# Kernel tuning notes

Hardware: AMD Instinct MI355X
Metric: run time of the kernel (lower is better)

Reference implementation:

```python
import jax, jax.numpy as jnp
import numpy as np

N_NODES = 100000
N_EDGES = 1600000
D_IN, D_HID, D_OUT = 128, 64, 16


def _glorot(key, shape):
    lim = float(np.sqrt(6.0 / (shape[0] + shape[1])))
    return jax.random.uniform(key, shape, jnp.float32, -lim, lim)


def setup_inputs() -> dict:
    key = jax.random.key(0)
    k1, k2, k3 = jax.random.split(key, 3)
    x = jax.random.normal(k1, (N_NODES, D_IN), dtype=jnp.float32)
    edge_index = jax.random.randint(k2, (2, N_EDGES), 0, N_NODES, dtype=jnp.int64)
    kw1, kw2 = jax.random.split(k3)
    W1 = _glorot(kw1, (D_IN, D_HID))
    b1 = jnp.zeros((D_HID,), jnp.float32)
    W2 = _glorot(kw2, (D_HID, D_OUT))
    b2 = jnp.zeros((D_OUT,), jnp.float32)
    return {"x": x, "edge_index": edge_index, "W1": W1, "b1": b1, "W2": W2, "b2": b2}


def _gcn_conv(h, W, b, src, dst, norm, n_nodes):
    # PyG GCNConv: linear first, then normalized neighbor aggregation, then bias.
    h = h @ W                                        # [N, d_out]
    msg = h[src] * norm[:, None]                     # gather over edges(+self loops)
    out = jax.ops.segment_sum(msg, dst, num_segments=n_nodes)  # scatter-add
    return out + b


def reference(x, edge_index, W1, b1, W2, b2):
    n = x.shape[0]
    loop = jnp.arange(n, dtype=edge_index.dtype)
    src = jnp.concatenate([edge_index[0], loop])     # add self loops
    dst = jnp.concatenate([edge_index[1], loop])
    # symmetric normalization D^-1/2 (A+I) D^-1/2
    deg = jax.ops.segment_sum(jnp.ones(src.shape[0], x.dtype), dst, num_segments=n)
    dinv = jnp.where(deg > 0, jax.lax.rsqrt(jnp.maximum(deg, 1e-12)), 0.0)
    norm = dinv[src] * dinv[dst]                     # [E+N]

    out = _gcn_conv(x, W1, b1, src, dst, norm, n)
    out = jax.nn.sigmoid(out)
    # dropout p=0.5 with training=False -> identity (eval mode)
    out = _gcn_conv(out, W2, b2, src, dst, norm, n)
    return jax.nn.log_softmax(out, axis=1)
```

## Files before the change

### kernel.cpp

```cpp
#include <hip/hip_runtime.h>
#include <hip/hip_bf16.h>


constexpr int D_IN  = 128;
constexpr int D_HID = 64;
constexpr int D_OUT = 16;

constexpr int WSHIFT  = 9;
constexpr int MAXB    = 256;
constexpr int BCAP    = 12288;
constexpr int CSRCAP  = 16384;
constexpr int BIN_CAP = 48;
constexpr int CHUNK   = 4096;

typedef __attribute__((ext_vector_type(8))) short bf16x8;
typedef __attribute__((ext_vector_type(4))) float f32x4;

__device__ inline float bflo(unsigned u){ return __uint_as_float(u << 16); }
__device__ inline float bfhi(unsigned u){ return __uint_as_float(u & 0xffff0000u); }
__device__ inline unsigned f2bu(float f){
    __hip_bfloat16 h = __float2bfloat16(f);
    return (unsigned)*reinterpret_cast<unsigned short*>(&h);
}
__device__ inline float sigf(float x){ return 1.0f / (1.0f + __expf(-x)); }

__global__ __launch_bounds__(256) void k_bucketize(
    const int* __restrict__ ei, const unsigned* __restrict__ xraw,
    int* __restrict__ flags, unsigned* __restrict__ gcur,
    unsigned* __restrict__ gbuf, int ne, int B)
{
    __shared__ unsigned bcnt[MAXB];
    __shared__ unsigned bbase[MAXB];
    __shared__ unsigned bins[MAXB * BIN_CAP];
    __shared__ int s_i64;

    const int t = threadIdx.x, lane = t & 63, wv = t >> 6;
    const int e0 = blockIdx.x * CHUNK;

    if (t < MAXB) bcnt[t] = 0u;
    if (wv == 0){
        int w = ei[2 * lane + 1];
        unsigned long long m = __ballot(w == 0);
        if (lane == 0) s_i64 = (__popcll(m) > 48) ? 1 : 0;
        if (blockIdx.x == 0){
            unsigned u = xraw[lane];
            unsigned h0 = u & 0xffffu, h1 = u >> 16;
            unsigned ex0 = (h0 >> 7) & 0xffu, ex1 = (h1 >> 7) & 0xffu;
            bool bad0 = !((h0 & 0x7fffu) == 0 || (ex0 >= 97 && ex0 <= 157));
            bool bad1 = !((h1 & 0x7fffu) == 0 || (ex1 >= 97 && ex1 <= 157));
            unsigned long long m0 = __ballot(bad0);
            unsigned long long m1 = __ballot(bad1);
            if (lane == 0){
                int bad = __popcll(m0) + __popcll(m1);
                flags[0] = (bad > 8) ? 0 : 1;
                flags[1] = s_i64;
            }
        }
    }
    __syncthreads();
    const int i64 = s_i64;
    const bool vec = ((ne & 1) == 0);

    #pragma unroll
    for (int k = 0; k < CHUNK / 512; ++k){
        int e = e0 + k * 512 + 2 * t;
        int s0, d0, s1, d1;
        int cntE = 0;
        if (vec && e < ne){
            if (i64){
                int4 sp = *(const int4*)&ei[2 * e];
                int4 dp = *(const int4*)&ei[2 * (ne + e)];
                s0 = sp.x; s1 = sp.z; d0 = dp.x; d1 = dp.z;
            } else {
                int2 sp = *(const int2*)&ei[e];
                int2 dp = *(const int2*)&ei[ne + e];
                s0 = sp.x; s1 = sp.y; d0 = dp.x; d1 = dp.y;
            }
            cntE = 2;
        } else {
            if (e < ne){
                if (i64){ s0 = ei[2*e]; d0 = ei[2*(ne+e)]; }
                else    { s0 = ei[e];   d0 = ei[ne+e]; }
                cntE = 1;
                if (e + 1 < ne){
                    if (i64){ s1 = ei[2*(e+1)]; d1 = ei[2*(ne+e+1)]; }
                    else    { s1 = ei[e+1];     d1 = ei[ne+e+1]; }
                    cntE = 2;
                }
            }
        }
        #pragma unroll
        for (int j = 0; j < 2; ++j){
            if (j < cntE){
                int s = j ? s1 : s0, d = j ? d1 : d0;
                int b = d >> WSHIFT;
                unsigned v = ((unsigned)s << WSHIFT) | ((unsigned)d & ((1u << WSHIFT) - 1));
                unsigned p = atomicAdd(&bcnt[b], 1u);
                if (p < (unsigned)BIN_CAP){
                    bins[b * BIN_CAP + p] = v;
                } else {
                    unsigned g = atomicAdd(&gcur[b], 1u);
                    gbuf[(size_t)b * BCAP + g] = v;
                }
            }
        }
    }
    __syncthreads();

    if (t < B){
        unsigned c = min(bcnt[t], (unsigned)BIN_CAP);
        bbase[t] = atomicAdd(&gcur[t], c);
    }
    __syncthreads();

    for (int b = wv; b < B; b += 4){
        unsigned c = min(bcnt[b], (unsigned)BIN_CAP);
        for (unsigned o = lane; o < c; o += 64)
            gbuf[(size_t)b * BCAP + bbase[b] + o] = bins[b * BIN_CAP + o];
    }
}

__global__ __launch_bounds__(1024) void k_build(
    const unsigned* __restrict__ gbuf, const unsigned* __restrict__ gcnt,
    unsigned* __restrict__ off, unsigned* __restrict__ offend,
    float* __restrict__ dinv, int* __restrict__ csr, int n, int B)
{
    __shared__ unsigned hist[512];
    __shared__ unsigned offl[512];
    __shared__ unsigned wsums[8];

    const int t = threadIdx.x, lane = t & 63, wv = t >> 6;
    const int b = blockIdx.x;
    const int base = b << WSHIFT;
    const int nodes = min(512, n - base);
    const unsigned bb = (unsigned)b * CSRCAP;

    if (t < 512) hist[t] = 0u;
    __syncthreads();
    const unsigned cnt = gcnt[b];
    const unsigned* mybuf = gbuf + (size_t)b * BCAP;

    for (unsigned i = t; i < cnt; i += 1024)
        atomicAdd(&hist[mybuf[i] & ((1u << WSHIFT) - 1)], 1u);
    __syncthreads();

    unsigned v = 0, p = 0, x = 0;
    if (t < 512){
        v = hist[t];
        p = (v + 7u) & ~7u;
        x = p;
        #pragma unroll
        for (int o = 1; o < 64; o <<= 1){
            unsigned y = __shfl_up(x, o, 64);
            if (lane >= o) x += y;
        }
        if (lane == 63) wsums[wv] = x;
    }
    __syncthreads();
    if (t == 0){
        unsigned run = 0;
        #pragma unroll
        for (int w = 0; w < 8; ++w){ unsigned tv = wsums[w]; wsums[w] = run; run += tv; }
    }
    __syncthreads();
    if (t < 512) offl[t] = x - p + wsums[wv];
    __syncthreads();

    if (t < nodes){
        off[base + t]    = bb + offl[t];
        offend[base + t] = bb + offl[t] + p;
        dinv[base + t]   = rsqrtf(1.0f + (float)v);
    }
    __syncthreads();

    if (t < 512) hist[t] = offl[t];
    __syncthreads();

    for (unsigned i = t; i < cnt; i += 1024){
        unsigned rec = mybuf[i];
        unsigned pos = atomicAdd(&hist[rec & ((1u << WSHIFT) - 1)], 1u);
        csr[bb + pos] = (int)(rec >> WSHIFT);
    }
    __syncthreads();

    if (t < nodes){
        unsigned s = offl[t] + v, e2 = offl[t] + p;
        for (unsigned j = s; j < e2; ++j) csr[bb + j] = n;
    }
}

__global__ __launch_bounds__(256) void k_linear1(
    const unsigned* __restrict__ xraw, const unsigned* __restrict__ w1raw,
    const int* __restrict__ flags, const float* __restrict__ dinv,
    unsigned short* __restrict__ h1s, int n)
{
    const int lane = threadIdx.x & 63;
    const int wv   = threadIdx.x >> 6;
    const int m = lane & 15, q = lane >> 4;
    const int isBf16 = flags[0];

    if (blockIdx.x == 0 && threadIdx.x < 16)
        ((uint2*)(h1s + (size_t)n * D_HID))[threadIdx.x] = make_uint2(0u, 0u);

    bf16x8 bfr[4][4];
    if (isBf16){
        const unsigned short* w = (const unsigned short*)w1raw;
        #pragma unroll
        for (int kc = 0; kc < 4; ++kc)
            #pragma unroll
            for (int ct = 0; ct < 4; ++ct)
                #pragma unroll
                for (int j = 0; j < 8; ++j)
                    bfr[kc][ct][j] = (short)w[(kc*32 + q*8 + j) * D_HID + ct*16 + m];
    } else {
        const float* w = (const float*)w1raw;
        #pragma unroll
        for (int kc = 0; kc < 4; ++kc)
            #pragma unroll
            for (int ct = 0; ct < 4; ++ct)
                #pragma unroll
                for (int j = 0; j < 8; ++j)
                    bfr[kc][ct][j] = (short)f2bu(w[(kc*32 + q*8 + j) * D_HID + ct*16 + m]);
    }

    const int ntiles = (n + 15) >> 4;
    for (int tile = blockIdx.x * 4 + wv; tile < ntiles; tile += gridDim.x * 4){
        const int node0 = tile << 4;
        int arow = node0 + m; if (arow >= n) arow = n - 1;
        f32x4 ac0 = {0,0,0,0}, ac1 = {0,0,0,0}, ac2 = {0,0,0,0}, ac3 = {0,0,0,0};
        #pragma unroll
        for (int kc = 0; kc < 4; ++kc){
            bf16x8 a;
            if (isBf16){
                uint4 u = *(const uint4*)((const unsigned short*)xraw + (size_t)arow * D_IN + kc*32 + q*8);
                a = *reinterpret_cast<bf16x8*>(&u);
            } else {
                const float* xp = (const float*)xraw + (size_t)arow * D_IN + kc*32 + q*8;
                float4 f0 = *(const float4*)xp;
                float4 f1 = *(const float4*)(xp + 4);
                a[0]=(short)f2bu(f0.x); a[1]=(short)f2bu(f0.y); a[2]=(short)f2bu(f0.z); a[3]=(short)f2bu(f0.w);
                a[4]=(short)f2bu(f1.x); a[5]=(short)f2bu(f1.y); a[6]=(short)f2bu(f1.z); a[7]=(short)f2bu(f1.w);
            }
            ac0 = __builtin_amdgcn_mfma_f32_16x16x32_bf16(a, bfr[kc][0], ac0, 0, 0, 0);
            ac1 = __builtin_amdgcn_mfma_f32_16x16x32_bf16(a, bfr[kc][1], ac1, 0, 0, 0);
            ac2 = __builtin_amdgcn_mfma_f32_16x16x32_bf16(a, bfr[kc][2], ac2, 0, 0, 0);
            ac3 = __builtin_amdgcn_mfma_f32_16x16x32_bf16(a, bfr[kc][3], ac3, 0, 0, 0);
        }
        #pragma unroll
        for (int i = 0; i < 4; ++i){
            int nr = node0 + q*4 + i;
            if (nr < n){
                float di = dinv[nr];
                unsigned short* o = h1s + (size_t)nr * D_HID + m;
                o[0]  = (unsigned short)f2bu(ac0[i] * di);
                o[16] = (unsigned short)f2bu(ac1[i] * di);
                o[32] = (unsigned short)f2bu(ac2[i] * di);
                o[48] = (unsigned short)f2bu(ac3[i] * di);
            }
        }
    }
}

__global__ __launch_bounds__(256) void k_aggA(
    const unsigned* __restrict__ off, const unsigned* __restrict__ offend,
    const int* __restrict__ csr_src,
    const float* __restrict__ dinv, const unsigned short* __restrict__ h1s,
    const unsigned* __restrict__ b1raw, const unsigned* __restrict__ w2raw,
    const int* __restrict__ flags,
    unsigned short* __restrict__ h2s, int n)
{
    __shared__ unsigned short act_s[16][72];

    const int lane = threadIdx.x & 63;
    const int wv   = threadIdx.x >> 6;
    const int grp  = lane >> 4;
    const int f    = lane & 15;
    const int dl   = wv * 4 + grp;
    const int d    = blockIdx.x * 16 + dl;
    const int isBf16 = flags[0];

    bf16x8 w2f[2];
    if (wv == 0){
        const int m0 = lane & 15, q0 = lane >> 4;
        if (isBf16){
            const unsigned short* w = (const unsigned short*)w2raw;
            #pragma unroll
            for (int kc = 0; kc < 2; ++kc)
                #pragma unroll
                for (int j = 0; j < 8; ++j)
                    w2f[kc][j] = (short)w[(kc*32 + q0*8 + j) * D_OUT + m0];
        } else {
            const float* w = (const float*)w2raw;
            #pragma unroll
            for (int kc = 0; kc < 2; ++kc)
                #pragma unroll
                for (int j = 0; j < 8; ++j)
                    w2f[kc][j] = (short)f2bu(w[(kc*32 + q0*8 + j) * D_OUT + m0]);
        }
        if (blockIdx.x == 0 && lane < 4)
            ((uint2*)(h2s + (size_t)n * D_OUT))[lane] = make_uint2(0u, 0u);
    }

    if (d < n){
        const int beg = (int)off[d], end = (int)offend[d];
        float a0=0.f, a1=0.f, a2=0.f, a3=0.f;
        for (int i = beg; i < end; i += 8){
            uint4 cA = *(const uint4*)&csr_src[i];
            uint4 cB = *(const uint4*)&csr_src[i + 4];
            uint2 u0 = *(const uint2*)&h1s[(size_t)(unsigned)cA.x * D_HID + f * 4];
            uint2 u1 = *(const uint2*)&h1s[(size_t)(unsigned)cA.y * D_HID + f * 4];
            uint2 u2 = *(const uint2*)&h1s[(size_t)(unsigned)cA.z * D_HID + f * 4];
            uint2 u3 = *(const uint2*)&h1s[(size_t)(unsigned)cA.w * D_HID + f * 4];
            uint2 u4 = *(const uint2*)&h1s[(size_t)(unsigned)cB.x * D_HID + f * 4];
            uint2 u5 = *(const uint2*)&h1s[(size_t)(unsigned)cB.y * D_HID + f * 4];
            uint2 u6 = *(const uint2*)&h1s[(size_t)(unsigned)cB.z * D_HID + f * 4];
            uint2 u7 = *(const uint2*)&h1s[(size_t)(unsigned)cB.w * D_HID + f * 4];
            a0 += bflo(u0.x) + bflo(u1.x) + bflo(u2.x) + bflo(u3.x)
                + bflo(u4.x) + bflo(u5.x) + bflo(u6.x) + bflo(u7.x);
            a1 += bfhi(u0.x) + bfhi(u1.x) + bfhi(u2.x) + bfhi(u3.x)
                + bfhi(u4.x) + bfhi(u5.x) + bfhi(u6.x) + bfhi(u7.x);
            a2 += bflo(u0.y) + bflo(u1.y) + bflo(u2.y) + bflo(u3.y)
                + bflo(u4.y) + bflo(u5.y) + bflo(u6.y) + bflo(u7.y);
            a3 += bfhi(u0.y) + bfhi(u1.y) + bfhi(u2.y) + bfhi(u3.y)
                + bfhi(u4.y) + bfhi(u5.y) + bfhi(u6.y) + bfhi(u7.y);
        }
        uint2 su = *(const uint2*)&h1s[(size_t)d * D_HID + f * 4];
        a0 += bflo(su.x); a1 += bfhi(su.x);
        a2 += bflo(su.y); a3 += bfhi(su.y);
        const float dd = dinv[d];
        float b0, b1v, b2v, b3v;
        if (isBf16){
            uint2 bu = ((const uint2*)b1raw)[f];
            b0 = bflo(bu.x); b1v = bfhi(bu.x); b2v = bflo(bu.y); b3v = bfhi(bu.y);
        } else {
            float4 bb = ((const float4*)b1raw)[f];
            b0 = bb.x; b1v = bb.y; b2v = bb.z; b3v = bb.w;
        }
        act_s[dl][f*4+0] = (unsigned short)f2bu(sigf(fmaf(a0, dd, b0)));
        act_s[dl][f*4+1] = (unsigned short)f2bu(sigf(fmaf(a1, dd, b1v)));
        act_s[dl][f*4+2] = (unsigned short)f2bu(sigf(fmaf(a2, dd, b2v)));
        act_s[dl][f*4+3] = (unsigned short)f2bu(sigf(fmaf(a3, dd, b3v)));
    } else {
        #pragma unroll
        for (int j = 0; j < 4; ++j) act_s[dl][f*4+j] = 0;
    }
    __syncthreads();

    if (wv == 0){
        const int m0 = lane & 15, q0 = lane >> 4;
        f32x4 acc = {0,0,0,0};
        #pragma unroll
        for (int kc = 0; kc < 2; ++kc){
            bf16x8 a;
            #pragma unroll
            for (int j = 0; j < 8; ++j)
                a[j] = (short)act_s[m0][kc*32 + q0*8 + j];
            acc = __builtin_amdgcn_mfma_f32_16x16x32_bf16(a, w2f[kc], acc, 0, 0, 0);
        }
        #pragma unroll
        for (int i = 0; i < 4; ++i){
            int nr = blockIdx.x * 16 + q0*4 + i;
            if (nr < n)
                h2s[(size_t)nr * D_OUT + m0] = (unsigned short)f2bu(acc[i] * dinv[nr]);
        }
    }
}

__global__ __launch_bounds__(256) void k_aggB(
    const unsigned* __restrict__ off, const unsigned* __restrict__ offend,
    const int* __restrict__ csr_src,
    const float* __restrict__ dinv, const unsigned short* __restrict__ h2s,
    const unsigned* __restrict__ b2raw, const int* __restrict__ flags,
    void* __restrict__ out, int n)
{
    const int lane = threadIdx.x & 63;
    const int wv   = threadIdx.x >> 6;
    const int grp  = lane >> 2;
    const int f    = lane & 3;
    const int d    = (blockIdx.x * 4 + wv) * 16 + grp;
    const int isBf16 = flags[0];
    if (d >= n) return;

    const int beg = (int)off[d], end = (int)offend[d];
    float a0=0.f, a1=0.f, a2=0.f, a3=0.f;
    for (int i = beg; i < end; i += 8){
        uint4 cA = *(const uint4*)&csr_src[i];
        uint4 cB = *(const uint4*)&csr_src[i + 4];
        uint2 u0 = *(const uint2*)&h2s[(size_t)(unsigned)cA.x * D_OUT + f * 4];
        uint2 u1 = *(const uint2*)&h2s[(size_t)(unsigned)cA.y * D_OUT + f * 4];
        uint2 u2 = *(const uint2*)&h2s[(size_t)(unsigned)cA.z * D_OUT + f * 4];
        uint2 u3 = *(const uint2*)&h2s[(size_t)(unsigned)cA.w * D_OUT + f * 4];
        uint2 u4 = *(const uint2*)&h2s[(size_t)(unsigned)cB.x * D_OUT + f * 4];
        uint2 u5 = *(const uint2*)&h2s[(size_t)(unsigned)cB.y * D_OUT + f * 4];
        uint2 u6 = *(const uint2*)&h2s[(size_t)(unsigned)cB.z * D_OUT + f * 4];
        uint2 u7 = *(const uint2*)&h2s[(size_t)(unsigned)cB.w * D_OUT + f * 4];
        a0 += bflo(u0.x) + bflo(u1.x) + bflo(u2.x) + bflo(u3.x)
            + bflo(u4.x) + bflo(u5.x) + bflo(u6.x) + bflo(u7.x);
        a1 += bfhi(u0.x) + bfhi(u1.x) + bfhi(u2.x) + bfhi(u3.x)
            + bfhi(u4.x) + bfhi(u5.x) + bfhi(u6.x) + bfhi(u7.x);
        a2 += bflo(u0.y) + bflo(u1.y) + bflo(u2.y) + bflo(u3.y)
            + bflo(u4.y) + bflo(u5.y) + bflo(u6.y) + bflo(u7.y);
        a3 += bfhi(u0.y) + bfhi(u1.y) + bfhi(u2.y) + bfhi(u3.y)
            + bfhi(u4.y) + bfhi(u5.y) + bfhi(u6.y) + bfhi(u7.y);
    }
    uint2 su = *(const uint2*)&h2s[(size_t)d * D_OUT + f * 4];
    a0 += bflo(su.x); a1 += bfhi(su.x);
    a2 += bflo(su.y); a3 += bfhi(su.y);
    const float dd = dinv[d];
    float b0, b1v, b2v, b3v;
    if (isBf16){
        uint2 bu = ((const uint2*)b2raw)[f];
        b0 = bflo(bu.x); b1v = bfhi(bu.x); b2v = bflo(bu.y); b3v = bfhi(bu.y);
    } else {
        float4 bb = ((const float4*)b2raw)[f];
        b0 = bb.x; b1v = bb.y; b2v = bb.z; b3v = bb.w;
    }
    a0 = fmaf(a0, dd, b0); a1 = fmaf(a1, dd, b1v);
    a2 = fmaf(a2, dd, b2v); a3 = fmaf(a3, dd, b3v);
    float m = fmaxf(fmaxf(a0, a1), fmaxf(a2, a3));
    m = fmaxf(m, __shfl_xor(m, 1, 4));
    m = fmaxf(m, __shfl_xor(m, 2, 4));
    float s = __expf(a0 - m) + __expf(a1 - m) + __expf(a2 - m) + __expf(a3 - m);
    s += __shfl_xor(s, 1, 4);
    s += __shfl_xor(s, 2, 4);
    float ls = m + __logf(s);
    if (isBf16){
        uint2 pk;
        pk.x = f2bu(a0 - ls) | (f2bu(a1 - ls) << 16);
        pk.y = f2bu(a2 - ls) | (f2bu(a3 - ls) << 16);
        *(uint2*)((__hip_bfloat16*)out + (size_t)d * D_OUT + f * 4) = pk;
    } else {
        float4 o4 = make_float4(a0 - ls, a1 - ls, a2 - ls, a3 - ls);
        *(float4*)((float*)out + (size_t)d * D_OUT + f * 4) = o4;
    }
}

extern "C" void kernel_launch(void* const* d_in, const int* in_sizes, int n_in,
                              void* d_out, int out_size, void* d_ws, size_t ws_size,
                              hipStream_t stream)
{
    const unsigned* xraw  = (const unsigned*)d_in[0];
    const int*      ei    = (const int*)d_in[1];
    const unsigned* w1raw = (const unsigned*)d_in[2];
    const unsigned* b1raw = (const unsigned*)d_in[3];
    const unsigned* w2raw = (const unsigned*)d_in[4];
    const unsigned* b2raw = (const unsigned*)d_in[5];

    const int n  = in_sizes[0] / D_IN;
    const int ne = in_sizes[1] / 2;
    const int B  = (n + ((1 << WSHIFT) - 1)) >> WSHIFT;

    size_t nAl = ((size_t)n + 255) & ~(size_t)255;
    int*            flags  = (int*)d_ws;
    unsigned*       gcur   = (unsigned*)d_ws + 64;
    float*          dinv   = (float*)(gcur + 256);
    unsigned*       off    = (unsigned*)(dinv + nAl);
    unsigned*       offend = off + nAl;
    int*            csr    = (int*)(offend + nAl);
    unsigned*       gbuf   = (unsigned*)(csr + (size_t)MAXB * CSRCAP);
    unsigned short* h1s    = (unsigned short*)(gbuf + (size_t)MAXB * BCAP);
    unsigned short* h2s    = h1s + (size_t)(n + 16) * D_HID;

    const int nchunk  = (ne + CHUNK - 1) / CHUNK;
    const int ntiles1 = (n + 15) / 16;
    const int grid1   = (ntiles1 + 3) / 4;

    hipMemsetAsync(gcur, 0, MAXB * sizeof(unsigned), stream);
    k_bucketize <<<nchunk, 256, 0, stream>>>(ei, xraw, flags, gcur, gbuf, ne, B);
    k_build     <<<B, 1024, 0, stream>>>(gbuf, gcur, off, offend, dinv, csr, n, B);

    k_linear1   <<<grid1, 256, 0, stream>>>(xraw, w1raw, flags, dinv, h1s, n);
    k_aggA      <<<(n + 15) / 16, 256, 0, stream>>>(off, offend, csr, dinv, h1s, b1raw, w2raw, flags, h2s, n);
    k_aggB      <<<(n + 63) / 64, 256, 0, stream>>>(off, offend, csr, dinv, h2s, b2raw, flags, d_out, n);
}
```

Baseline: 194.6 us.

## Fuse first-layer linear transform into CSR build kernel and shrink bucketize chunks

```diff
diff --git a/kernel.cpp b/kernel.cpp
--- a/kernel.cpp
+++ b/kernel.cpp
@@ -10,8 +10,8 @@
 constexpr int MAXB    = 256;
 constexpr int BCAP    = 12288;
 constexpr int CSRCAP  = 16384;
-constexpr int BIN_CAP = 48;
-constexpr int CHUNK   = 4096;
+constexpr int BIN_CAP = 24;
+constexpr int CHUNK   = 2048;
 
 typedef __attribute__((ext_vector_type(8))) short bf16x8;
 typedef __attribute__((ext_vector_type(4))) float f32x4;
@@ -115,19 +115,24 @@
 
     for (int b = wv; b < B; b += 4){
         unsigned c = min(bcnt[b], (unsigned)BIN_CAP);
+        unsigned ba = bbase[b];
         for (unsigned o = lane; o < c; o += 64)
-            gbuf[(size_t)b * BCAP + bbase[b] + o] = bins[b * BIN_CAP + o];
-    }
-}
-
-__global__ __launch_bounds__(1024) void k_build(
+            gbuf[(size_t)b * BCAP + ba + o] = bins[b * BIN_CAP + o];
+    }
+}
+
+__global__ __launch_bounds__(1024, 4) void k_build_lin1(
     const unsigned* __restrict__ gbuf, const unsigned* __restrict__ gcnt,
     unsigned* __restrict__ off, unsigned* __restrict__ offend,
-    float* __restrict__ dinv, int* __restrict__ csr, int n, int B)
+    float* __restrict__ dinv, int* __restrict__ csr,
+    const unsigned* __restrict__ xraw, const unsigned* __restrict__ w1raw,
+    const int* __restrict__ flags, unsigned short* __restrict__ h1s,
+    int n, int B)
 {
     __shared__ unsigned hist[512];
     __shared__ unsigned offl[512];
     __shared__ unsigned wsums[8];
+    __shared__ float    s_dinv[512];
 
     const int t = threadIdx.x, lane = t & 63, wv = t >> 6;
     const int b = blockIdx.x;
@@ -167,9 +172,11 @@
     __syncthreads();
 
     if (t < nodes){
+        float dv = rsqrtf(1.0f + (float)v);
         off[base + t]    = bb + offl[t];
         offend[base + t] = bb + offl[t] + p;
-        dinv[base + t]   = rsqrtf(1.0f + (float)v);
+        dinv[base + t]   = dv;
+        s_dinv[t]        = dv;
     }
     __syncthreads();
 
@@ -187,45 +194,16 @@
         unsigned s = offl[t] + v, e2 = offl[t] + p;
         for (unsigned j = s; j < e2; ++j) csr[bb + j] = n;
     }
-}
-
-__global__ __launch_bounds__(256) void k_linear1(
-    const unsigned* __restrict__ xraw, const unsigned* __restrict__ w1raw,
-    const int* __restrict__ flags, const float* __restrict__ dinv,
-    unsigned short* __restrict__ h1s, int n)
-{
-    const int lane = threadIdx.x & 63;
-    const int wv   = threadIdx.x >> 6;
+    __syncthreads();
+
+    const int isBf16 = flags[0];
+    if (b == 0 && t < 16)
+        ((uint2*)(h1s + (size_t)n * D_HID))[t] = make_uint2(0u, 0u);
+
     const int m = lane & 15, q = lane >> 4;
-    const int isBf16 = flags[0];
-
-    if (blockIdx.x == 0 && threadIdx.x < 16)
-        ((uint2*)(h1s + (size_t)n * D_HID))[threadIdx.x] = make_uint2(0u, 0u);
-
-    bf16x8 bfr[4][4];
-    if (isBf16){
-        const unsigned short* w = (const unsigned short*)w1raw;
-        #pragma unroll
-        for (int kc = 0; kc < 4; ++kc)
-            #pragma unroll
-            for (int ct = 0; ct < 4; ++ct)
-                #pragma unroll
-                for (int j = 0; j < 8; ++j)
-                    bfr[kc][ct][j] = (short)w[(kc*32 + q*8 + j) * D_HID + ct*16 + m];
-    } else {
-        const float* w = (const float*)w1raw;
-        #pragma unroll
-        for (int kc = 0; kc < 4; ++kc)
-            #pragma unroll
-            for (int ct = 0; ct < 4; ++ct)
-                #pragma unroll
-                for (int j = 0; j < 8; ++j)
-                    bfr[kc][ct][j] = (short)f2bu(w[(kc*32 + q*8 + j) * D_HID + ct*16 + m]);
-    }
-
-    const int ntiles = (n + 15) >> 4;
-    for (int tile = blockIdx.x * 4 + wv; tile < ntiles; tile += gridDim.x * 4){
-        const int node0 = tile << 4;
+    const int ntb = (nodes + 15) >> 4;
+    for (int tt = wv; tt < ntb; tt += 16){
+        const int node0 = base + (tt << 4);
         int arow = node0 + m; if (arow >= n) arow = n - 1;
         f32x4 ac0 = {0,0,0,0}, ac1 = {0,0,0,0}, ac2 = {0,0,0,0}, ac3 = {0,0,0,0};
         #pragma unroll
@@ -241,16 +219,34 @@
                 a[0]=(short)f2bu(f0.x); a[1]=(short)f2bu(f0.y); a[2]=(short)f2bu(f0.z); a[3]=(short)f2bu(f0.w);
                 a[4]=(short)f2bu(f1.x); a[5]=(short)f2bu(f1.y); a[6]=(short)f2bu(f1.z); a[7]=(short)f2bu(f1.w);
             }
-            ac0 = __builtin_amdgcn_mfma_f32_16x16x32_bf16(a, bfr[kc][0], ac0, 0, 0, 0);
-            ac1 = __builtin_amdgcn_mfma_f32_16x16x32_bf16(a, bfr[kc][1], ac1, 0, 0, 0);
-            ac2 = __builtin_amdgcn_mfma_f32_16x16x32_bf16(a, bfr[kc][2], ac2, 0, 0, 0);
-            ac3 = __builtin_amdgcn_mfma_f32_16x16x32_bf16(a, bfr[kc][3], ac3, 0, 0, 0);
+            bf16x8 b0, b1, b2, b3;
+            if (isBf16){
+                const unsigned short* w = (const unsigned short*)w1raw;
+                #pragma unroll
+                for (int j = 0; j < 8; ++j){
+                    int r = (kc*32 + q*8 + j) * D_HID + m;
+                    b0[j] = (short)w[r];      b1[j] = (short)w[r + 16];
+                    b2[j] = (short)w[r + 32]; b3[j] = (short)w[r + 48];
+                }
+            } else {
+                const float* w = (const float*)w1raw;
+                #pragma unroll
+                for (int j = 0; j < 8; ++j){
+                    int r = (kc*32 + q*8 + j) * D_HID + m;
+                    b0[j] = (short)f2bu(w[r]);      b1[j] = (short)f2bu(w[r + 16]);
+                    b2[j] = (short)f2bu(w[r + 32]); b3[j] = (short)f2bu(w[r + 48]);
+                }
+            }
+            ac0 = __builtin_amdgcn_mfma_f32_16x16x32_bf16(a, b0, ac0, 0, 0, 0);
+            ac1 = __builtin_amdgcn_mfma_f32_16x16x32_bf16(a, b1, ac1, 0, 0, 0);
+            ac2 = __builtin_amdgcn_mfma_f32_16x16x32_bf16(a, b2, ac2, 0, 0, 0);
+            ac3 = __builtin_amdgcn_mfma_f32_16x16x32_bf16(a, b3, ac3, 0, 0, 0);
         }
         #pragma unroll
         for (int i = 0; i < 4; ++i){
             int nr = node0 + q*4 + i;
             if (nr < n){
-                float di = dinv[nr];
+                float di = s_dinv[nr - base];
                 unsigned short* o = h1s + (size_t)nr * D_HID + m;
                 o[0]  = (unsigned short)f2bu(ac0[i] * di);
                 o[16] = (unsigned short)f2bu(ac1[i] * di);
@@ -461,15 +457,12 @@
     unsigned short* h1s    = (unsigned short*)(gbuf + (size_t)MAXB * BCAP);
     unsigned short* h2s    = h1s + (size_t)(n + 16) * D_HID;
 
-    const int nchunk  = (ne + CHUNK - 1) / CHUNK;
-    const int ntiles1 = (n + 15) / 16;
-    const int grid1   = (ntiles1 + 3) / 4;
+    const int nchunk = (ne + CHUNK - 1) / CHUNK;
 
     hipMemsetAsync(gcur, 0, MAXB * sizeof(unsigned), stream);
-    k_bucketize <<<nchunk, 256, 0, stream>>>(ei, xraw, flags, gcur, gbuf, ne, B);
-    k_build     <<<B, 1024, 0, stream>>>(gbuf, gcur, off, offend, dinv, csr, n, B);
-
-    k_linear1   <<<grid1, 256, 0, stream>>>(xraw, w1raw, flags, dinv, h1s, n);
-    k_aggA      <<<(n + 15) / 16, 256, 0, stream>>>(off, offend, csr, dinv, h1s, b1raw, w2raw, flags, h2s, n);
-    k_aggB      <<<(n + 63) / 64, 256, 0, stream>>>(off, offend, csr, dinv, h2s, b2raw, flags, d_out, n);
-}
+    k_bucketize  <<<nchunk, 256, 0, stream>>>(ei, xraw, flags, gcur, gbuf, ne, B);
+    k_build_lin1 <<<B, 1024, 0, stream>>>(gbuf, gcur, off, offend, dinv, csr,
+                                          xraw, w1raw, flags, h1s, n, B);
+    k_aggA       <<<(n + 15) / 16, 256, 0, stream>>>(off, offend, csr, dinv, h1s, b1raw, w2raw, flags, h2s, n);
+    k_aggB       <<<(n + 63) / 64, 256, 0, stream>>>(off, offend, csr, dinv, h2s, b2raw, flags, d_out, n);
+}
```

Result: slower. 377.2 us (+93.8%).
